# Kernel tuning notes

Hardware: AMD Instinct MI355X
Metric: run time of the kernel (lower is better)

The kernel has to match this reference:

```python
import jax, jax.numpy as jnp
import numpy as np

KS = 3          # kernel_size
PAD = 1         # padding (reflect)
RATIO = 0.5     # offset scale


def setup_inputs() -> dict:
    key = jax.random.key(0)
    x = jax.random.normal(key, (8, 64, 128, 128), dtype=jnp.float32)
    return {"x": x}


def _sampling_grid(h, w, hp, wp):
    """Returns float coords px[h,1,N], py[1,w,N] and clipped int corner indices."""
    ks = KS
    r = jnp.arange(-(ks - 1) // 2, (ks - 1) // 2 + 1, dtype=jnp.float32)
    dx, dy = jnp.meshgrid(r, r, indexing='ij')      # kernel offsets, row-major (dx, dy)
    dx = dx.reshape(-1)                             # [N]
    dy = dy.reshape(-1)                             # [N]
    px = (jnp.arange(h, dtype=jnp.float32) + ks // 2)[:, None, None] + dx * RATIO  # [h,1,N]
    py = (jnp.arange(w, dtype=jnp.float32) + ks // 2)[None, :, None] + dy * RATIO  # [1,w,N]
    qx0 = jnp.floor(px)
    qy0 = jnp.floor(py)
    qx1 = qx0 + 1.0
    qy1 = qy0 + 1.0
    ix0 = jnp.clip(qx0.astype(jnp.int32), 0, hp - 1)
    ix1 = jnp.clip(qx1.astype(jnp.int32), 0, hp - 1)
    iy0 = jnp.clip(qy0.astype(jnp.int32), 0, wp - 1)
    iy1 = jnp.clip(qy1.astype(jnp.int32), 0, wp - 1)
    # bilinear weights (match torch: g_lt=(1+(q0-p)), g_rb=(1-(q1-p)), etc.)
    gx0 = 1.0 + (qx0 - px)   # [h,1,N]
    gx1 = 1.0 - (qx1 - px)
    gy0 = 1.0 + (qy0 - py)   # [1,w,N]
    gy1 = 1.0 - (qy1 - py)
    return (ix0, ix1, iy0, iy1, gx0, gx1, gy0, gy1)


def reference(x):
    b, c, h, w = x.shape
    ks = KS
    xp = jnp.pad(x, ((0, 0), (0, 0), (PAD, PAD), (PAD, PAD)), mode='reflect')
    hp, wp = h + 2 * PAD, w + 2 * PAD
    ix0, ix1, iy0, iy1, gx0, gx1, gy0, gy1 = _sampling_grid(h, w, hp, wp)
    # 4-corner gather; index arrays broadcast to [h,w,N] -> result [b,c,h,w,N]
    x_lt = xp[:, :, ix0, iy0]
    x_rb = xp[:, :, ix1, iy1]
    x_lb = xp[:, :, ix0, iy1]
    x_rt = xp[:, :, ix1, iy0]
    x_off = (gx0 * gy0) * x_lt + (gx1 * gy1) * x_rb + (gx0 * gy1) * x_lb + (gx1 * gy0) * x_rt
    # _reshape_x_offset: [b,c,h,w,N=ks*ks] -> [b,c,h*ks,w*ks]
    out = x_off.reshape(b, c, h, w, ks, ks)        # N split as (dx, dy)
    out = out.transpose(0, 1, 2, 4, 3, 5)          # [b,c,h,dx,w,dy]
    return out.reshape(b, c, h * ks, w * ks)
```

## Files before the change

### kernel.cpp

```cpp
#include <hip/hip_runtime.h>


namespace {

constexpr int H  = 128, W  = 128;
constexpr int HO = 384, WO = 384;

typedef float f32x4 __attribute__((ext_vector_type(4)));

__global__ __launch_bounds__(256) void rf_scale_kernel(const float* __restrict__ x,
                                                       float* __restrict__ out) {
    __shared__ float lds[8 * WO];

    const int tid    = threadIdx.x;
    const int g      = tid & 31;
    const int lr     = tid >> 5;
    const int rowgrp = blockIdx.x;
    const int bc     = blockIdx.y;

    const int ho = rowgrp * 8 + lr;
    const int h  = ho / 3;
    const int i  = ho - h * 3;

    int r0 = h, r1 = h;
    if (i == 0)      r0 = (h == 0)     ? 1     : h - 1;
    else if (i == 2) r1 = (h == H - 1) ? H - 2 : h + 1;

    const float* base = x + (size_t)bc * (H * W);
    const int wb = g << 2;

    f32x4 a0 = *(const f32x4*)(base + r0 * W + wb);
    f32x4 a1 = *(const f32x4*)(base + r1 * W + wb);

    float R1 = a0.x + a1.x;
    float R2 = a0.y + a1.y;
    float R3 = a0.z + a1.z;
    float R4 = a0.w + a1.w;

    float Rm = __shfl_up(R4, 1);
    float Rp = __shfl_down(R1, 1);
    float R0 = (g == 0)  ? R2 : Rm;
    float R5 = (g == 31) ? R3 : Rp;

    float e01 = 0.25f * (R0 + R1);
    float e12 = 0.25f * (R1 + R2);
    float e23 = 0.25f * (R2 + R3);
    float e34 = 0.25f * (R3 + R4);
    float e45 = 0.25f * (R4 + R5);

    f32x4 o0 = {e01,       0.5f * R1, e12,       e12      };
    f32x4 o1 = {0.5f * R2, e23,       e23,       0.5f * R3};
    f32x4 o2 = {e34,       e34,       0.5f * R4, e45      };

    float* lp = lds + lr * WO + g * 12;
    ((f32x4*)lp)[0] = o0;
    ((f32x4*)lp)[1] = o1;
    ((f32x4*)lp)[2] = o2;

    const int wv = tid >> 6;
    const int ln = tid & 63;
    const int b0 = wv * 192 + ln;

    const f32x4* ls = (const f32x4*)lds;
    f32x4* op = (f32x4*)(out + ((size_t)bc * HO + (size_t)rowgrp * 8) * WO);
    __builtin_nontemporal_store(ls[b0],       &op[b0]);
    __builtin_nontemporal_store(ls[b0 + 64],  &op[b0 + 64]);
    __builtin_nontemporal_store(ls[b0 + 128], &op[b0 + 128]);
}

}

extern "C" void kernel_launch(void* const* d_in, const int* in_sizes, int n_in,
                              void* d_out, int out_size, void* d_ws, size_t ws_size,
                              hipStream_t stream) {
    const float* x = (const float*)d_in[0];
    float* out = (float*)d_out;

    int nbc = in_sizes[0] / (H * W);
    dim3 grid(HO / 8, nbc);
    rf_scale_kernel<<<grid, 256, 0, stream>>>(x, out);
}
```

Before: 312.0 us.

## Compute three output rows per input row to reuse loaded rows

Each thread now handles one input row and produces all three interpolated output rows from three loaded input rows (above, center, below). Before, each thread loaded two rows for a single output row. Each block now covers 24 output rows, so the grid shrinks threefold and global reads per output row drop. In exchange LDS per block triples to 36 KB, which may reduce occupancy, and each thread issues more stores.

```diff
diff --git a/kernel.cpp b/kernel.cpp
--- a/kernel.cpp
+++ b/kernel.cpp
@@ -8,64 +8,78 @@
 
 typedef float f32x4 __attribute__((ext_vector_type(4)));
 
+__device__ __forceinline__ void emit12(float* lp, float S0, float S1, float S2,
+                                       float S3, float S4, float S5,
+                                       float we, float wc) {
+    float e01 = we * (S0 + S1);
+    float e12 = we * (S1 + S2);
+    float e23 = we * (S2 + S3);
+    float e34 = we * (S3 + S4);
+    float e45 = we * (S4 + S5);
+    f32x4 o0 = {e01,     wc * S1, e12,     e12    };
+    f32x4 o1 = {wc * S2, e23,     e23,     wc * S3};
+    f32x4 o2 = {e34,     e34,     wc * S4, e45    };
+    ((f32x4*)lp)[0] = o0;
+    ((f32x4*)lp)[1] = o1;
+    ((f32x4*)lp)[2] = o2;
+}
+
 __global__ __launch_bounds__(256) void rf_scale_kernel(const float* __restrict__ x,
                                                        float* __restrict__ out) {
-    __shared__ float lds[8 * WO];
+    __shared__ float lds[24 * WO];
 
-    const int tid    = threadIdx.x;
-    const int g      = tid & 31;
-    const int lr     = tid >> 5;
-    const int rowgrp = blockIdx.x;
-    const int bc     = blockIdx.y;
+    const int tid = threadIdx.x;
+    const int g   = tid & 31;
+    const int hl  = tid >> 5;
+    const int bx  = blockIdx.x;
+    const int bc  = blockIdx.y;
 
-    const int ho = rowgrp * 8 + lr;
-    const int h  = ho / 3;
-    const int i  = ho - h * 3;
-
-    int r0 = h, r1 = h;
-    if (i == 0)      r0 = (h == 0)     ? 1     : h - 1;
-    else if (i == 2) r1 = (h == H - 1) ? H - 2 : h + 1;
+    const int h  = bx * 8 + hl;
+    const int rm = (h == 0)     ? 1     : h - 1;
+    const int rp = (h == H - 1) ? H - 2 : h + 1;
 
     const float* base = x + (size_t)bc * (H * W);
     const int wb = g << 2;
 
-    f32x4 a0 = *(const f32x4*)(base + r0 * W + wb);
-    f32x4 a1 = *(const f32x4*)(base + r1 * W + wb);
+    f32x4 xm = *(const f32x4*)(base + rm * W + wb);
+    f32x4 x0 = *(const f32x4*)(base + h  * W + wb);
+    f32x4 xp = *(const f32x4*)(base + rp * W + wb);
 
-    float R1 = a0.x + a1.x;
-    float R2 = a0.y + a1.y;
-    float R3 = a0.z + a1.z;
-    float R4 = a0.w + a1.w;
+    float* lp = lds + (3 * hl) * WO + g * 12;
 
-    float Rm = __shfl_up(R4, 1);
-    float Rp = __shfl_down(R1, 1);
-    float R0 = (g == 0)  ? R2 : Rm;
-    float R5 = (g == 31) ? R3 : Rp;
-
-    float e01 = 0.25f * (R0 + R1);
-    float e12 = 0.25f * (R1 + R2);
-    float e23 = 0.25f * (R2 + R3);
-    float e34 = 0.25f * (R3 + R4);
-    float e45 = 0.25f * (R4 + R5);
-
-    f32x4 o0 = {e01,       0.5f * R1, e12,       e12      };
-    f32x4 o1 = {0.5f * R2, e23,       e23,       0.5f * R3};
-    f32x4 o2 = {e34,       e34,       0.5f * R4, e45      };
-
-    float* lp = lds + lr * WO + g * 12;
-    ((f32x4*)lp)[0] = o0;
-    ((f32x4*)lp)[1] = o1;
-    ((f32x4*)lp)[2] = o2;
+    {
+        float A1 = xm.x + x0.x, A2 = xm.y + x0.y, A3 = xm.z + x0.z, A4 = xm.w + x0.w;
+        float Am = __shfl_up(A4, 1);
+        float Ap = __shfl_down(A1, 1);
+        float A0 = (g == 0)  ? A2 : Am;
+        float A5 = (g == 31) ? A3 : Ap;
+        emit12(lp, A0, A1, A2, A3, A4, A5, 0.25f, 0.5f);
+    }
+    {
+        float Bm = __shfl_up(x0.w, 1);
+        float Bp = __shfl_down(x0.x, 1);
+        float B0 = (g == 0)  ? x0.y : Bm;
+        float B5 = (g == 31) ? x0.z : Bp;
+        emit12(lp + WO, B0, x0.x, x0.y, x0.z, x0.w, B5, 0.5f, 1.0f);
+    }
+    {
+        float C1 = x0.x + xp.x, C2 = x0.y + xp.y, C3 = x0.z + xp.z, C4 = x0.w + xp.w;
+        float Cm = __shfl_up(C4, 1);
+        float Cp = __shfl_down(C1, 1);
+        float C0 = (g == 0)  ? C2 : Cm;
+        float C5 = (g == 31) ? C3 : Cp;
+        emit12(lp + 2 * WO, C0, C1, C2, C3, C4, C5, 0.25f, 0.5f);
+    }
 
     const int wv = tid >> 6;
     const int ln = tid & 63;
-    const int b0 = wv * 192 + ln;
+    const int b0 = wv * 576 + ln;
 
     const f32x4* ls = (const f32x4*)lds;
-    f32x4* op = (f32x4*)(out + ((size_t)bc * HO + (size_t)rowgrp * 8) * WO);
-    __builtin_nontemporal_store(ls[b0],       &op[b0]);
-    __builtin_nontemporal_store(ls[b0 + 64],  &op[b0 + 64]);
-    __builtin_nontemporal_store(ls[b0 + 128], &op[b0 + 128]);
+    f32x4* op = (f32x4*)(out + ((size_t)bc * HO + (size_t)bx * 24) * WO);
+#pragma unroll
+    for (int k = 0; k < 9; ++k)
+        __builtin_nontemporal_store(ls[b0 + 64 * k], &op[b0 + 64 * k]);
 }
 
 }
@@ -77,6 +91,6 @@
     float* out = (float*)d_out;
 
     int nbc = in_sizes[0] / (H * W);
-    dim3 grid(HO / 8, nbc);
+    dim3 grid(H / 8, nbc);
     rf_scale_kernel<<<grid, 256, 0, stream>>>(x, out);
 }
```

After: 310.0 us. About the same (-0.6%).
